# Optimization experiments

Hardware: AMD Instinct MI355X
Metric: run time of the kernel (lower is better)

Reference implementation:

```python
import math
import jax, jax.numpy as jnp
import numpy as np

N_HEADS, INPUT_DIM, EMBED_DIM = 8, 512, 512
KEY_DIM = EMBED_DIM // N_HEADS  # 64, val_dim == key_dim
BATCH, N = 4, 2048


def setup_inputs() -> dict:
    key = jax.random.key(0)
    ks = jax.random.split(key, 6)
    def unif(k, shape):
        stdv = 1.0 / math.sqrt(shape[-1])
        return jax.random.uniform(k, shape, jnp.float32, -stdv, stdv)
    q = jax.random.normal(ks[0], (BATCH, N, INPUT_DIM), jnp.float32)
    mask = jax.random.randint(ks[1], (BATCH, N, N), 0, 2, jnp.int32)
    W_query = unif(ks[2], (N_HEADS, INPUT_DIM, KEY_DIM))
    W_key = unif(ks[3], (N_HEADS, INPUT_DIM, KEY_DIM))
    W_val = unif(ks[4], (N_HEADS, INPUT_DIM, KEY_DIM))
    W_out = unif(ks[5], (N_HEADS, KEY_DIM, EMBED_DIM))
    return {"q": q, "mask": mask, "W_query": W_query, "W_key": W_key,
            "W_val": W_val, "W_out": W_out}


def reference(q, mask, W_query, W_key, W_val, W_out):
    # Self-attention: k is None, v is None -> k = q, v = q (module forward_).
    norm = 1.0 / math.sqrt(KEY_DIM)
    m = mask.astype(bool)[None]  # (1, b, nq, ng) broadcast over heads
    Q = jnp.einsum('bnd,hdk->hbnk', q, W_query)  # (h, b, nq, dk)
    K = jnp.einsum('bnd,hdk->hbnk', q, W_key)    # (h, b, ng, dk)
    V = jnp.einsum('bnd,hdv->hbnv', q, W_val)    # (h, b, ng, dv)
    scores = norm * jnp.einsum('hbqk,hbgk->hbqg', Q, K)  # (h, b, nq, ng)
    scores = jnp.where(m, -jnp.inf, scores)
    attn = jax.nn.softmax(scores, axis=-1)
    attn = jnp.where(m, 0.0, attn)  # zero out masked (also kills NaN rows)
    heads = jnp.einsum('hbqg,hbgv->hbqv', attn, V)
    out = jnp.einsum('hbqv,hve->bqe', heads, W_out)  # (b, nq, embed)
    return out
```

## Files before the change

kernel.cpp:

```cpp
#include <hip/hip_runtime.h>
#include <hip/hip_bf16.h>
#include <stdint.h>

using bf16 = __hip_bfloat16;
typedef __attribute__((ext_vector_type(8))) short short8;
typedef __attribute__((ext_vector_type(4))) short short4b;
typedef __attribute__((ext_vector_type(4))) float f32x4;
typedef __attribute__((ext_vector_type(4))) unsigned int u32x4;

#if __has_builtin(__builtin_amdgcn_exp2f)
#define EXP2(x) __builtin_amdgcn_exp2f(x)
#else
#define EXP2(x) exp2f(x)
#endif

__device__ __forceinline__ short8 load8(const bf16* p) {
  return *reinterpret_cast<const short8*>(p);
}
__device__ __forceinline__ short f2b(float f) {
  return __builtin_bit_cast(short, __float2bfloat16(f));
}
__device__ __forceinline__ unsigned int pk2(float a, float b) {
  return (unsigned int)(unsigned short)f2b(a) |
         ((unsigned int)(unsigned short)f2b(b) << 16);
}
__device__ __forceinline__ void asy16(const bf16* g, bf16* l) {
  __builtin_amdgcn_global_load_lds(
      (const __attribute__((address_space(1))) void*)g,
      (__attribute__((address_space(3))) void*)l, 16, 0, 0);
}


__global__ void k_prep(const float4* __restrict__ x, ushort4* __restrict__ xb,
                       const float* __restrict__ Wq, const float* __restrict__ Wk,
                       const float* __restrict__ Wv, const float* __restrict__ Wo,
                       bf16* __restrict__ Wcat, bf16* __restrict__ Wot,
                       const int4* __restrict__ m4,
                       unsigned long long* __restrict__ bits) {
  int blk = blockIdx.x;
  const int tid = threadIdx.x;
  if (blk < 4096) {
    int i = blk * 256 + tid;
    float4 v = x[i];
    ushort4 o;
    o.x = (unsigned short)f2b(v.x);
    o.y = (unsigned short)f2b(v.y);
    o.z = (unsigned short)f2b(v.z);
    o.w = (unsigned short)f2b(v.w);
    xb[i] = o;
  } else if (blk < 4352) {
    int t = blk - 4096;
    __shared__ float T[64][65];
    if (t < 192) {
      int which = t >> 6;
      int h = (t >> 3) & 7, dt = t & 7;
      const float* W = (which == 0) ? Wq : ((which == 1) ? Wk : Wv);
#pragma unroll
      for (int p = 0; p < 4; ++p) {
        int row = p * 16 + (tid >> 4);
        float4 v = *(const float4*)(W + (size_t)(h * 512 + dt * 64 + row) * 64 +
                                    (tid & 15) * 4);
        T[row][(tid & 15) * 4 + 0] = v.x;
        T[row][(tid & 15) * 4 + 1] = v.y;
        T[row][(tid & 15) * 4 + 2] = v.z;
        T[row][(tid & 15) * 4 + 3] = v.w;
      }
      __syncthreads();
      float scale = (which == 0) ? 0.18033688011112042f : 1.0f;
      int jj = tid >> 2, i0 = (tid & 3) * 16;
#pragma unroll
      for (int q = 0; q < 2; ++q) {
        short8 o;
#pragma unroll
        for (int e = 0; e < 8; ++e) o[e] = f2b(T[i0 + q * 8 + e][jj] * scale);
        *(short8*)(Wcat + (size_t)(which * 512 + h * 64 + jj) * 512 + dt * 64 +
                   i0 + q * 8) = o;
      }
    } else {
      int t2 = t - 192;
      int h = t2 >> 3, et = t2 & 7;
#pragma unroll
      for (int p = 0; p < 4; ++p) {
        int row = p * 16 + (tid >> 4);
        float4 v = *(const float4*)(Wo + (size_t)(h * 64 + row) * 512 + et * 64 +
                                    (tid & 15) * 4);
        T[row][(tid & 15) * 4 + 0] = v.x;
        T[row][(tid & 15) * 4 + 1] = v.y;
        T[row][(tid & 15) * 4 + 2] = v.z;
        T[row][(tid & 15) * 4 + 3] = v.w;
      }
      __syncthreads();
      int jj = tid >> 2, i0 = (tid & 3) * 16;
#pragma unroll
      for (int q = 0; q < 2; ++q) {
        short8 o;
#pragma unroll
        for (int e = 0; e < 8; ++e) o[e] = f2b(T[i0 + q * 8 + e][jj]);
        *(short8*)(Wot + (size_t)(et * 64 + jj) * 512 + h * 64 + i0 + q * 8) = o;
      }
    }
  } else {
    int i = (blk - 4352) * 256 + tid;
    int4 v = m4[i];
    unsigned int nib = (unsigned)(v.x != 0) | ((unsigned)(v.y != 0) << 1) |
                       ((unsigned)(v.z != 0) << 2) | ((unsigned)(v.w != 0) << 3);
    unsigned long long w = (unsigned long long)nib << (4 * (tid & 15));
    w |= __shfl_xor(w, 1);
    w |= __shfl_xor(w, 2);
    w |= __shfl_xor(w, 4);
    w |= __shfl_xor(w, 8);
    if ((tid & 15) == 0) bits[i >> 4] = w;
  }
}

__device__ __forceinline__ void gemm128(const bf16* __restrict__ A,
                                        const bf16* __restrict__ Bt,
                                        bf16* As, bf16* Bs,
                                        int rowBase, int colBase,
                                        f32x4 acc[4][4]) {
  const int tid = threadIdx.x;
  const int lane = tid & 63, w = tid >> 6;
  const int g = lane >> 4, r = lane & 15;

  auto stage = [&](int buf, int s) {
#pragma unroll
    for (int p = 0; p < 2; ++p) {
      int c = p * 256 + tid;
      int row = c >> 2, gr = c & 3, sg = gr ^ (row & 3);
      asy16(A + (size_t)(rowBase + row) * 512 + s * 32 + sg * 8,
            As + buf * 4096 + c * 8);
    }
#pragma unroll
    for (int p = 0; p < 2; ++p) {
      int c = p * 256 + tid;
      int row = c >> 2, gr = c & 3, sg = gr ^ (row & 3);
      asy16(Bt + (size_t)(colBase + row) * 512 + s * 32 + sg * 8,
            Bs + buf * 4096 + c * 8);
    }
  };

  stage(0, 0);
  int buf = 0;
  const int rbl = (w >> 1) * 64, cbl = (w & 1) * 64;
  for (int s = 0; s < 16; ++s) {
    __syncthreads();
    if (s < 15) stage(buf ^ 1, s + 1);
    const bf16* a0 = As + buf * 4096;
    const bf16* b0 = Bs + buf * 4096;
    short8 af[4], bfr[4];
#pragma unroll
    for (int mt = 0; mt < 4; ++mt) {
      int row = rbl + mt * 16 + r;
      af[mt] = load8(a0 + (row * 4 + (g ^ (row & 3))) * 8);
    }
#pragma unroll
    for (int nt = 0; nt < 4; ++nt) {
      int col = cbl + nt * 16 + r;
      bfr[nt] = load8(b0 + (col * 4 + (g ^ (col & 3))) * 8);
    }
#pragma unroll
    for (int mt = 0; mt < 4; ++mt)
#pragma unroll
      for (int nt = 0; nt < 4; ++nt)
        acc[mt][nt] = __builtin_amdgcn_mfma_f32_16x16x32_bf16(
            af[mt], bfr[nt], acc[mt][nt], 0, 0, 0);
    buf ^= 1;
  }
}

__global__ __launch_bounds__(256, 3) void k_proj_qkv(
    const bf16* __restrict__ Xb, const bf16* __restrict__ Wcat,
    bf16* __restrict__ Qb, bf16* __restrict__ Kp, bf16* __restrict__ Vp) {
  __shared__ __align__(16) bf16 As[2 * 4096];
  __shared__ __align__(16) bf16 Bs[2 * 4096];
  int rowBase = blockIdx.x * 128, colBase = blockIdx.y * 128;
  f32x4 acc[4][4] = {};
  gemm128(Xb, Wcat, As, Bs, rowBase, colBase, acc);
  const int lane = threadIdx.x & 63, w = threadIdx.x >> 6;
  const int g = lane >> 4, r = lane & 15;
#pragma unroll
  for (int mt = 0; mt < 4; ++mt) {
    int row0 = rowBase + (w >> 1) * 64 + mt * 16 + 4 * g;
    int b = row0 >> 11, n0 = row0 & 2047;
    int kt = n0 >> 6;
#pragma unroll
    for (int nt = 0; nt < 4; ++nt) {
      int col = colBase + (w & 1) * 64 + nt * 16 + r;
      if (col < 512) {
        int hh = col >> 6, dk = col & 63;
        bf16* p0 = Qb + ((size_t)(b * 8 + hh) * 2048 + n0) * 64 + dk;
#pragma unroll
        for (int rr = 0; rr < 4; ++rr)
          p0[rr * 64] = __float2bfloat16(acc[mt][nt][rr]);
      } else if (col < 1024) {
        int hh = (col >> 6) & 7, dk = col & 63;
        int half = dk >> 5, gk = (dk >> 3) & 3, jj = dk & 7;
        int kr = n0 & 63;
        int kc = kr >> 4, r0 = kr & 15;
        bf16* base = Kp + (size_t)(b * 8 + hh) * 131072 + (size_t)kt * 4096 +
                     ((kc * 2 + half) * 4 + gk) * 128 + jj;
#pragma unroll
        for (int rr = 0; rr < 4; ++rr)
          base[(r0 + rr) * 8] = __float2bfloat16(acc[mt][nt][rr]);
      } else {
        int hdv = col - 1024;
        int hh = hdv >> 6, dv = hdv & 63;
        int dvs = dv >> 4, rv = dv & 15;
        int kcol0 = n0 & 63;
        int half = kcol0 >> 5, gv = (kcol0 >> 2) & 3;
        int j0 = ((kcol0 >> 4) & 1) * 4;
        short4b pkv;
#pragma unroll
        for (int rr = 0; rr < 4; ++rr) pkv[rr] = f2b(acc[mt][nt][rr]);
        *reinterpret_cast<short4b*>(
            Vp + (size_t)(b * 8 + hh) * 131072 + (size_t)kt * 4096 +
            (((half * 4 + dvs) * 4 + gv) * 16 + rv) * 8 + j0) = pkv;
      }
    }
  }
}

__global__ __launch_bounds__(256, 2) void k_proj_out(
    const bf16* __restrict__ O, const bf16* __restrict__ Wot,
    float* __restrict__ out) {
  __shared__ __align__(16) bf16 As[2 * 4096];
  __shared__ __align__(16) bf16 Bs[2 * 4096];
  int rowBase = blockIdx.x * 128, colBase = blockIdx.y * 128;
  f32x4 acc[4][4] = {};
  gemm128(O, Wot, As, Bs, rowBase, colBase, acc);
  const int lane = threadIdx.x & 63, w = threadIdx.x >> 6;
  const int g = lane >> 4, r = lane & 15;
#pragma unroll
  for (int mt = 0; mt < 4; ++mt) {
    int row0 = rowBase + (w >> 1) * 64 + mt * 16 + 4 * g;
#pragma unroll
    for (int nt = 0; nt < 4; ++nt) {
      int col = colBase + (w & 1) * 64 + nt * 16 + r;
#pragma unroll
      for (int rr = 0; rr < 4; ++rr)
        out[(size_t)(row0 + rr) * 512 + col] = acc[mt][nt][rr];
    }
  }
}

__global__ __launch_bounds__(512, 4) void k_attn(const bf16* __restrict__ Q,
    const bf16* __restrict__ K, const bf16* __restrict__ V,
    const unsigned long long* __restrict__ MB, bf16* __restrict__ O) {
  const int blin = blockIdx.x;
  const int j = blin >> 3;
  const int bh = (blin & 7) * 4 + (j >> 4);
  const int qt = j & 15;
  const int b = bh >> 3, h = bh & 7;
  const int tid = threadIdx.x;
  const int lane = tid & 63;
  const int wave = tid >> 6;
  const int g = lane >> 4, r = lane & 15;
  const int qbase = qt * 128 + wave * 16;

  __shared__ __align__(16) bf16 Kl[3][4096];
  __shared__ __align__(16) bf16 Vl[3][4096];

  const bf16* Kp = K + (size_t)bh * 131072;
  const bf16* Vp = V + (size_t)bh * 131072;

  short8 qf0, qf1;
  {
    const bf16* Qp = Q + ((size_t)bh * 2048 + qbase + r) * 64;
    qf0 = load8(Qp + g * 8);
    qf1 = load8(Qp + 32 + g * 8);
  }
  const unsigned long long* Mp = MB + ((size_t)b * 2048 + qbase + r) * 32;

  short8 ones;
#pragma unroll
  for (int i = 0; i < 8; ++i) ones[i] = (short)0x3F80;

  f32x4 acc[4] = {};
  f32x4 acc_l = {};

  auto stage = [&](int buf, int kt) {
    const bf16* Kg = Kp + (size_t)kt * 4096;
    const bf16* Vg = Vp + (size_t)kt * 4096;
    asy16(Kg + tid * 8, &Kl[buf][0] + tid * 8);
    asy16(Vg + tid * 8, &Vl[buf][0] + tid * 8);
  };

  auto qk = [&](const bf16* kl, f32x4 stl[4]) {
#pragma unroll
    for (int kc = 0; kc < 4; ++kc) {
      short8 kf0 = load8(kl + ((kc * 2 + 0) * 4 + g) * 128 + r * 8);
      short8 kf1 = load8(kl + ((kc * 2 + 1) * 4 + g) * 128 + r * 8);
      f32x4 z = {};
      z = __builtin_amdgcn_mfma_f32_16x16x32_bf16(kf0, qf0, z, 0, 0, 0);
      stl[kc] = __builtin_amdgcn_mfma_f32_16x16x32_bf16(kf1, qf1, z, 0, 0, 0);
    }
  };

  stage(0, 0);
  stage(1, 1);
  unsigned long long mwc = Mp[0];
  __syncthreads();
  f32x4 st_cur[4];
  qk(&Kl[0][0], st_cur);

  int b_cur = 0, b_nxt = 1, b_st = 2;

  for (int kt = 0; kt < 32; ++kt) {
    __syncthreads();
    if (kt < 30) stage(b_st, kt + 2);
    unsigned long long mwn = 0;
    if (kt < 31) mwn = Mp[kt + 1];

    f32x4 stn[4];
    if (kt < 31) qk(&Kl[b_nxt][0], stn);

    unsigned ml = (unsigned)mwc >> (4 * g);
    unsigned mh = (unsigned)(mwc >> 32) >> (4 * g);
    float p[16];
#pragma unroll
    for (int kc = 0; kc < 4; ++kc)
#pragma unroll
      for (int rr = 0; rr < 4; ++rr) {
        float e = EXP2(st_cur[kc][rr]);
        unsigned wsel = (kc & 2) ? mh : ml;
        bool bad = (wsel >> (((kc & 1) << 4) + rr)) & 1u;
        p[kc * 4 + rr] = bad ? 0.f : e;
      }
    u32x4 q0, q1;
#pragma unroll
    for (int i2 = 0; i2 < 4; ++i2) {
      q0[i2] = pk2(p[2 * i2], p[2 * i2 + 1]);
      q1[i2] = pk2(p[8 + 2 * i2], p[8 + 2 * i2 + 1]);
    }
    short8 pa0 = __builtin_bit_cast(short8, q0);
    short8 pa1 = __builtin_bit_cast(short8, q1);
    acc_l = __builtin_amdgcn_mfma_f32_16x16x32_bf16(pa0, ones, acc_l, 0, 0, 0);
    acc_l = __builtin_amdgcn_mfma_f32_16x16x32_bf16(pa1, ones, acc_l, 0, 0, 0);

    const bf16* vl = &Vl[b_cur][0];
#pragma unroll
    for (int dvs = 0; dvs < 4; ++dvs) {
      short8 vb0 = load8(vl + ((0 * 4 + dvs) * 4 + g) * 128 + r * 8);
      short8 vb1 = load8(vl + ((1 * 4 + dvs) * 4 + g) * 128 + r * 8);
      acc[dvs] = __builtin_amdgcn_mfma_f32_16x16x32_bf16(pa0, vb0, acc[dvs], 0, 0, 0);
      acc[dvs] = __builtin_amdgcn_mfma_f32_16x16x32_bf16(pa1, vb1, acc[dvs], 0, 0, 0);
    }

#pragma unroll
    for (int kc = 0; kc < 4; ++kc) st_cur[kc] = stn[kc];
    mwc = mwn;
    int t = b_cur; b_cur = b_nxt; b_nxt = b_st; b_st = t;
  }

  float inv[4];
#pragma unroll
  for (int rr = 0; rr < 4; ++rr)
    inv[rr] = (acc_l[rr] > 0.f) ? 1.f / acc_l[rr] : 0.f;
  bf16* Op = O + ((size_t)b * 2048 + qbase + 4 * g) * 512 + h * 64;
#pragma unroll
  for (int dvs = 0; dvs < 4; ++dvs)
#pragma unroll
    for (int rr = 0; rr < 4; ++rr)
      Op[rr * 512 + dvs * 16 + r] = __float2bfloat16(acc[dvs][rr] * inv[rr]);
}


extern "C" void kernel_launch(void* const* d_in, const int* in_sizes, int n_in,
                              void* d_out, int out_size, void* d_ws, size_t ws_size,
                              hipStream_t stream) {
  const float* q    = (const float*)d_in[0];
  const int*   mask = (const int*)d_in[1];
  const float* Wq   = (const float*)d_in[2];
  const float* Wk   = (const float*)d_in[3];
  const float* Wv   = (const float*)d_in[4];
  const float* Wo   = (const float*)d_in[5];
  float* out = (float*)d_out;

  char* ws = (char*)d_ws;
  const size_t MB1 = 1024 * 1024;
  bf16* Xb   = (bf16*)(ws + 0);
  bf16* Qb   = (bf16*)(ws + 8 * MB1);
  bf16* Kpm  = (bf16*)(ws + 16 * MB1);
  bf16* Vpm  = (bf16*)(ws + 24 * MB1);
  bf16* Ob   = (bf16*)(ws + 32 * MB1);
  unsigned long long* Mbits = (unsigned long long*)(ws + 40 * MB1);
  bf16* Wcat = (bf16*)(ws + 42 * MB1);
  bf16* Wot  = (bf16*)(ws + 42 * MB1 + 1536 * 512 * 2);

  k_prep<<<20736, 256, 0, stream>>>((const float4*)q, (ushort4*)Xb,
                                    Wq, Wk, Wv, Wo, Wcat, Wot,
                                    (const int4*)mask, Mbits);
  k_proj_qkv<<<dim3(64, 12), 256, 0, stream>>>(Xb, Wcat, Qb, Kpm, Vpm);
  k_attn<<<512, 512, 0, stream>>>(Qb, Kpm, Vpm, Mbits, Ob);
  k_proj_out<<<dim3(64, 4), 256, 0, stream>>>(Ob, Wot, out);
}
```

Baseline: 203.9 us.

## Halve attention block size, split K/V staging, add priority hints

The attention kernel now runs 1024 blocks of 4 waves, each covering 64 queries, where before it ran 512 blocks of 8 waves covering 128. Shared buffers drop from triple to double, with K prefetched two tiles ahead and V one tile ahead. The loop is unrolled by two with fixed buffer indices, and s_setprio is raised around the MFMA sections. The aim is more resident blocks and better overlap of loads with compute, at the cost of each K/V tile being loaded from global memory by twice as many blocks.

```diff
diff --git a/kernel.cpp b/kernel.cpp
--- a/kernel.cpp
+++ b/kernel.cpp
@@ -243,22 +243,22 @@
   }
 }
 
-__global__ __launch_bounds__(512, 4) void k_attn(const bf16* __restrict__ Q,
+__global__ __launch_bounds__(256, 4) void k_attn(const bf16* __restrict__ Q,
     const bf16* __restrict__ K, const bf16* __restrict__ V,
     const unsigned long long* __restrict__ MB, bf16* __restrict__ O) {
   const int blin = blockIdx.x;
   const int j = blin >> 3;
-  const int bh = (blin & 7) * 4 + (j >> 4);
-  const int qt = j & 15;
+  const int bh = (blin & 7) * 4 + (j >> 5);
+  const int qt = j & 31;
   const int b = bh >> 3, h = bh & 7;
   const int tid = threadIdx.x;
   const int lane = tid & 63;
   const int wave = tid >> 6;
   const int g = lane >> 4, r = lane & 15;
-  const int qbase = qt * 128 + wave * 16;
-
-  __shared__ __align__(16) bf16 Kl[3][4096];
-  __shared__ __align__(16) bf16 Vl[3][4096];
+  const int qbase = qt * 64 + wave * 16;
+
+  __shared__ __align__(16) bf16 Kl[2][4096];
+  __shared__ __align__(16) bf16 Vl[2][4096];
 
   const bf16* Kp = K + (size_t)bh * 131072;
   const bf16* Vp = V + (size_t)bh * 131072;
@@ -278,11 +278,15 @@
   f32x4 acc[4] = {};
   f32x4 acc_l = {};
 
-  auto stage = [&](int buf, int kt) {
+  auto stageK = [&](int buf, int kt) {
     const bf16* Kg = Kp + (size_t)kt * 4096;
+    asy16(Kg + tid * 8, &Kl[buf][0] + tid * 8);
+    asy16(Kg + 2048 + tid * 8, &Kl[buf][0] + 2048 + tid * 8);
+  };
+  auto stageV = [&](int buf, int kt) {
     const bf16* Vg = Vp + (size_t)kt * 4096;
-    asy16(Kg + tid * 8, &Kl[buf][0] + tid * 8);
     asy16(Vg + tid * 8, &Vl[buf][0] + tid * 8);
+    asy16(Vg + 2048 + tid * 8, &Vl[buf][0] + 2048 + tid * 8);
   };
 
   auto qk = [&](const bf16* kl, f32x4 stl[4]) {
@@ -296,61 +300,62 @@
     }
   };
 
-  stage(0, 0);
-  stage(1, 1);
-  unsigned long long mwc = Mp[0];
+  stageK(0, 0);
+  stageK(1, 1);
+  stageV(0, 0);
+  unsigned long long mw0, mw1;
+  mw0 = Mp[0];
   __syncthreads();
-  f32x4 st_cur[4];
-  qk(&Kl[0][0], st_cur);
-
-  int b_cur = 0, b_nxt = 1, b_st = 2;
-
-  for (int kt = 0; kt < 32; ++kt) {
-    __syncthreads();
-    if (kt < 30) stage(b_st, kt + 2);
-    unsigned long long mwn = 0;
-    if (kt < 31) mwn = Mp[kt + 1];
-
-    f32x4 stn[4];
-    if (kt < 31) qk(&Kl[b_nxt][0], stn);
-
-    unsigned ml = (unsigned)mwc >> (4 * g);
-    unsigned mh = (unsigned)(mwc >> 32) >> (4 * g);
-    float p[16];
-#pragma unroll
-    for (int kc = 0; kc < 4; ++kc)
-#pragma unroll
-      for (int rr = 0; rr < 4; ++rr) {
-        float e = EXP2(st_cur[kc][rr]);
-        unsigned wsel = (kc & 2) ? mh : ml;
-        bool bad = (wsel >> (((kc & 1) << 4) + rr)) & 1u;
-        p[kc * 4 + rr] = bad ? 0.f : e;
-      }
-    u32x4 q0, q1;
-#pragma unroll
-    for (int i2 = 0; i2 < 4; ++i2) {
-      q0[i2] = pk2(p[2 * i2], p[2 * i2 + 1]);
-      q1[i2] = pk2(p[8 + 2 * i2], p[8 + 2 * i2 + 1]);
-    }
-    short8 pa0 = __builtin_bit_cast(short8, q0);
-    short8 pa1 = __builtin_bit_cast(short8, q1);
-    acc_l = __builtin_amdgcn_mfma_f32_16x16x32_bf16(pa0, ones, acc_l, 0, 0, 0);
-    acc_l = __builtin_amdgcn_mfma_f32_16x16x32_bf16(pa1, ones, acc_l, 0, 0, 0);
-
-    const bf16* vl = &Vl[b_cur][0];
-#pragma unroll
-    for (int dvs = 0; dvs < 4; ++dvs) {
-      short8 vb0 = load8(vl + ((0 * 4 + dvs) * 4 + g) * 128 + r * 8);
-      short8 vb1 = load8(vl + ((1 * 4 + dvs) * 4 + g) * 128 + r * 8);
-      acc[dvs] = __builtin_amdgcn_mfma_f32_16x16x32_bf16(pa0, vb0, acc[dvs], 0, 0, 0);
-      acc[dvs] = __builtin_amdgcn_mfma_f32_16x16x32_bf16(pa1, vb1, acc[dvs], 0, 0, 0);
-    }
-
-#pragma unroll
-    for (int kc = 0; kc < 4; ++kc) st_cur[kc] = stn[kc];
-    mwc = mwn;
-    int t = b_cur; b_cur = b_nxt; b_nxt = b_st; b_st = t;
-  }
+  f32x4 st0[4], st1[4];
+  qk(&Kl[0][0], st0);
+
+#define ATTN_ITER(KT, CUR, NXT, SC, SN, MC, MN)                              \
+  do {                                                                       \
+    __syncthreads();                                                         \
+    if ((KT) < 30) stageK(CUR, (KT) + 2);                                    \
+    if ((KT) < 31) {                                                         \
+      stageV(NXT, (KT) + 1);                                                 \
+      MN = Mp[(KT) + 1];                                                     \
+    }                                                                        \
+    __builtin_amdgcn_s_setprio(1);                                           \
+    if ((KT) < 31) qk(&Kl[NXT][0], SN);                                      \
+    __builtin_amdgcn_s_setprio(0);                                           \
+    unsigned ml = (unsigned)MC >> (4 * g);                                   \
+    unsigned mh = (unsigned)(MC >> 32) >> (4 * g);                           \
+    float p[16];                                                             \
+    _Pragma("unroll") for (int kc = 0; kc < 4; ++kc)                         \
+        _Pragma("unroll") for (int rr = 0; rr < 4; ++rr) {                   \
+      float e = EXP2(SC[kc][rr]);                                            \
+      unsigned wsel = (kc & 2) ? mh : ml;                                    \
+      bool bad = (wsel >> (((kc & 1) << 4) + rr)) & 1u;                      \
+      p[kc * 4 + rr] = bad ? 0.f : e;                                        \
+    }                                                                        \
+    u32x4 q0, q1;                                                            \
+    _Pragma("unroll") for (int i2 = 0; i2 < 4; ++i2) {                       \
+      q0[i2] = pk2(p[2 * i2], p[2 * i2 + 1]);                                \
+      q1[i2] = pk2(p[8 + 2 * i2], p[8 + 2 * i2 + 1]);                        \
+    }                                                                        \
+    short8 pa0 = __builtin_bit_cast(short8, q0);                             \
+    short8 pa1 = __builtin_bit_cast(short8, q1);                             \
+    acc_l = __builtin_amdgcn_mfma_f32_16x16x32_bf16(pa0, ones, acc_l, 0, 0, 0); \
+    acc_l = __builtin_amdgcn_mfma_f32_16x16x32_bf16(pa1, ones, acc_l, 0, 0, 0); \
+    const bf16* vl = &Vl[CUR][0];                                            \
+    __builtin_amdgcn_s_setprio(1);                                           \
+    _Pragma("unroll") for (int dvs = 0; dvs < 4; ++dvs) {                    \
+      short8 vb0 = load8(vl + ((0 * 4 + dvs) * 4 + g) * 128 + r * 8);        \
+      short8 vb1 = load8(vl + ((1 * 4 + dvs) * 4 + g) * 128 + r * 8);        \
+      acc[dvs] = __builtin_amdgcn_mfma_f32_16x16x32_bf16(pa0, vb0, acc[dvs], 0, 0, 0); \
+      acc[dvs] = __builtin_amdgcn_mfma_f32_16x16x32_bf16(pa1, vb1, acc[dvs], 0, 0, 0); \
+    }                                                                        \
+    __builtin_amdgcn_s_setprio(0);                                           \
+  } while (0)
+
+  for (int t = 0; t < 16; ++t) {
+    const int kt = 2 * t;
+    ATTN_ITER(kt, 0, 1, st0, st1, mw0, mw1);
+    ATTN_ITER(kt + 1, 1, 0, st1, st0, mw1, mw0);
+  }
+#undef ATTN_ITER
 
   float inv[4];
 #pragma unroll
@@ -391,6 +396,6 @@
                                     Wq, Wk, Wv, Wo, Wcat, Wot,
                                     (const int4*)mask, Mbits);
   k_proj_qkv<<<dim3(64, 12), 256, 0, stream>>>(Xb, Wcat, Qb, Kpm, Vpm);
-  k_attn<<<512, 512, 0, stream>>>(Qb, Kpm, Vpm, Mbits, Ob);
+  k_attn<<<1024, 256, 0, stream>>>(Qb, Kpm, Vpm, Mbits, Ob);
   k_proj_out<<<dim3(64, 4), 256, 0, stream>>>(Ob, Wot, out);
 }
```

Measured after the change: 207.2 us. Within noise of the previous version (+1.6%).
